# Optimization experiments

Measured on AMD Instinct MI355X. Metric: run time of the kernel, lower is better.

The kernel has to match this reference:

```python
import jax, jax.numpy as jnp
import numpy as np

N, E, G = 20000, 320000, 128
HID, HEADS, LAYERS, IN = 128, 4, 2, 74
EPS = 1e-5


def setup_inputs() -> dict:
    key = jax.random.key(0)
    ks = jax.random.split(key, 10)
    h = jax.random.normal(ks[0], (N, IN), dtype=jnp.float32)
    src = jax.random.randint(ks[1], (E,), 0, N, dtype=jnp.int32)
    dst = jax.random.randint(ks[2], (E,), 0, N, dtype=jnp.int32)
    graph_ids = jnp.sort(jax.random.randint(ks[3], (N,), 0, G, dtype=jnp.int32))
    W0 = jax.random.normal(ks[4], (HEADS, IN, HID), dtype=jnp.float32) / np.sqrt(IN)
    Wr = jax.random.normal(ks[5], (LAYERS - 1, HEADS, HID, HID), dtype=jnp.float32) / np.sqrt(HID)
    att = jax.random.normal(ks[6], (LAYERS, HEADS, 2 * HID), dtype=jnp.float32) / np.sqrt(2 * HID)
    gamma = jnp.ones((LAYERS, HEADS, HID), dtype=jnp.float32)
    beta = jnp.zeros((LAYERS, HEADS, HID), dtype=jnp.float32)
    out_w = jax.random.normal(ks[7], (LAYERS, HID), dtype=jnp.float32) / np.sqrt(HID)
    out_b = jnp.zeros((LAYERS,), dtype=jnp.float32)
    return {"h": h, "src": src, "dst": dst, "graph_ids": graph_ids,
            "W0": W0, "Wr": Wr, "att": att, "gamma": gamma, "beta": beta,
            "out_w": out_w, "out_b": out_b}


def _gat_head(h, W, a, g, b, src, dst):
    # h: [N, F_in], W: [F_in, HID], a: [2*HID]
    z = h @ W                                  # [N, HID]
    zs, zd = z[src], z[dst]                    # [E, HID] gathers
    e = jax.nn.leaky_relu(zs @ a[:HID] + zd @ a[HID:])  # [E] edge logits
    # segment softmax over incoming edges of each dst node
    emax = jax.ops.segment_max(e, dst, num_segments=N)
    ex = jnp.exp(e - emax[dst])
    denom = jax.ops.segment_sum(ex, dst, num_segments=N)
    alpha = ex / denom[dst]
    hout = jax.ops.segment_sum(alpha[:, None] * zs, dst, num_segments=N)  # [N, HID]
    r = jax.nn.relu(hout)
    # BatchNorm1d (training-mode batch stats, biased variance)
    mean = r.mean(0)
    var = r.var(0)
    return g * (r - mean) / jnp.sqrt(var + EPS) + b


def reference(h, src, dst, graph_ids, W0, Wr, att, gamma, beta, out_w, out_b):
    heads = jax.vmap(_gat_head, in_axes=(None, 0, 0, 0, 0, None, None))
    x = h
    for j in range(LAYERS):
        W = W0 if j == 0 else Wr[j - 1]
        hs = heads(x, W, att[j], gamma[j], beta[j], src, dst)  # [HEADS, N, HID]
        hs = jnp.transpose(hs, (1, 0, 2))                       # [N, HEADS, HID]
        score = jax.nn.softmax(hs @ out_w[j] + out_b[j], axis=1)  # [N, HEADS]
        x = jnp.einsum('nh,nhd->nd', score, hs)                 # [N, HID]
    # dgl.mean_nodes: per-graph mean of node features
    counts = jax.ops.segment_sum(jnp.ones((N,), dtype=x.dtype), graph_ids, num_segments=G)
    sums = jax.ops.segment_sum(x, graph_ids, num_segments=G)
    return sums / jnp.maximum(counts, 1.0)[:, None]
```

## Files before the change

kernel.cpp:

```cpp
#include <hip/hip_runtime.h>
#include <hip/hip_bf16.h>

typedef unsigned short u16;
typedef unsigned int u32;
typedef __attribute__((ext_vector_type(8))) short bf16x8;
typedef __attribute__((ext_vector_type(4))) float f32x4;

#define NN 20000
#define NE 320000
#define NG 128
#define HD 128
#define NH 4
#define KIN 74
#define KP0 96
#define BN_EPS 1e-5f

__device__ __forceinline__ float bf2f(u16 v){ return __uint_as_float(((u32)v)<<16); }
__device__ __forceinline__ float bflo(u32 v){ return __uint_as_float(v<<16); }
__device__ __forceinline__ float bfhi(u32 v){ return __uint_as_float(v & 0xffff0000u); }
__device__ __forceinline__ u16 f2bf(float f){
    u32 u = __float_as_uint(f);
    return (u16)((u + 0x7fffu + ((u>>16)&1u)) >> 16);
}
__device__ __forceinline__ u32 pack2(float a, float b){
    return (u32)f2bf(a) | ((u32)f2bf(b) << 16);
}

__global__ void k_hist(const int* __restrict__ dst, int* __restrict__ counts){
    int e = blockIdx.x*256 + threadIdx.x;
    if(e < NE) atomicAdd(&counts[dst[e]], 1);
}

__global__ void k_scan(const int* __restrict__ counts, int* __restrict__ rowptr,
                       int* __restrict__ cursor){
    __shared__ int wsum[16];
    int tx = threadIdx.x, lane = tx & 63, wid = tx >> 6;
    int running = 0;
    for(int t = 0; t < (NN + 1023)/1024; ++t){
        int i = t*1024 + tx;
        int v = (i < NN) ? counts[i] : 0;
        int s = v;
        #pragma unroll
        for(int d = 1; d < 64; d <<= 1){ int o = __shfl_up(s, d); if(lane >= d) s += o; }
        if(lane == 63) wsum[wid] = s;
        __syncthreads();
        int woff = 0, total = 0;
        for(int w_ = 0; w_ < 16; ++w_){ int sw = wsum[w_]; total += sw; if(w_ < wid) woff += sw; }
        int ex = running + woff + s - v;
        if(i < NN){ rowptr[i] = ex; cursor[i] = ex; }
        running += total;
        __syncthreads();
    }
    if(tx == 0) rowptr[NN] = running;
}

__global__ void k_scatter(const int* __restrict__ src, const int* __restrict__ dst,
                          int* __restrict__ cursor, int* __restrict__ srcs){
    int e = blockIdx.x*256 + threadIdx.x;
    if(e >= NE) return;
    int d = dst[e];
    int p = atomicAdd(&cursor[d], 1);
    srcs[p] = src[e];
}

__global__ void k_prep_h(const float* __restrict__ h, u16* __restrict__ hb){
    int i = blockIdx.x*256 + threadIdx.x;
    if(i >= NN*KP0) return;
    int n = i / KP0, k = i - n*KP0;
    hb[i] = (k < KIN) ? f2bf(h[n*KIN + k]) : (u16)0;
}

__global__ void k_prep_w0(const float* __restrict__ W0, u16* __restrict__ wt){
    int i = blockIdx.x*256 + threadIdx.x;
    if(i >= NH*HD*KP0) return;
    int k = i % KP0; int c = (i/KP0) % HD; int h = i/(KP0*HD);
    wt[i] = (k < KIN) ? f2bf(W0[(h*KIN + k)*HD + c]) : (u16)0;
}

__global__ void k_prep_w1(const float* __restrict__ Wr, u16* __restrict__ wt){
    int i = blockIdx.x*256 + threadIdx.x;
    if(i >= NH*HD*HD) return;
    int k = i % HD; int c = (i/HD) % HD; int h = i/(HD*HD);
    wt[i] = f2bf(Wr[(h*HD + k)*HD + c]);
}

template<int KP>
__global__ void k_gemm_mfma(const u16* __restrict__ xb, const u16* __restrict__ wt,
                            u16* __restrict__ z){
    int h = blockIdx.y;
    int tx = threadIdx.x, lane = tx & 63, w = tx >> 6;
    int n0 = blockIdx.x*32 + (w >> 1)*16;
    int c0 = (w & 1)*64;
    int r16 = lane & 15, kg = lane >> 4;
    const u16* ap = xb + (size_t)(n0 + r16)*KP + kg*8;
    const u16* bp = wt + ((size_t)h*HD + c0 + r16)*KP + kg*8;
    f32x4 acc0 = {0.f,0.f,0.f,0.f}, acc1 = {0.f,0.f,0.f,0.f};
    f32x4 acc2 = {0.f,0.f,0.f,0.f}, acc3 = {0.f,0.f,0.f,0.f};
    #pragma unroll
    for(int k0 = 0; k0 < KP; k0 += 32){
        bf16x8 av = *(const bf16x8*)(ap + k0);
        bf16x8 b0 = *(const bf16x8*)(bp + k0);
        bf16x8 b1 = *(const bf16x8*)(bp + 16*KP + k0);
        bf16x8 b2 = *(const bf16x8*)(bp + 32*KP + k0);
        bf16x8 b3 = *(const bf16x8*)(bp + 48*KP + k0);
        acc0 = __builtin_amdgcn_mfma_f32_16x16x32_bf16(av, b0, acc0, 0, 0, 0);
        acc1 = __builtin_amdgcn_mfma_f32_16x16x32_bf16(av, b1, acc1, 0, 0, 0);
        acc2 = __builtin_amdgcn_mfma_f32_16x16x32_bf16(av, b2, acc2, 0, 0, 0);
        acc3 = __builtin_amdgcn_mfma_f32_16x16x32_bf16(av, b3, acc3, 0, 0, 0);
    }
    int nbase = n0 + kg*4;
    u16* zp = z + ((size_t)nbase*NH + h)*HD + c0 + r16;
    #pragma unroll
    for(int reg = 0; reg < 4; ++reg){
        u16* q = zp + (size_t)reg*NH*HD;
        q[0]  = f2bf(acc0[reg]);
        q[16] = f2bf(acc1[reg]);
        q[32] = f2bf(acc2[reg]);
        q[48] = f2bf(acc3[reg]);
    }
}

__global__ void k_dots(const u16* __restrict__ z, const float* __restrict__ attj,
                       float* __restrict__ es, float* __restrict__ ed){
    int tx = threadIdx.x, lane = tx & 63, w = tx >> 6;
    int n = blockIdx.x*4 + w;
    if(n >= NN) return;
    int ch = lane*2;
    for(int h = 0; h < NH; ++h){
        u32 zz = *(const u32*)(z + (size_t)(n*NH + h)*HD + ch);
        float z0 = bflo(zz);
        float z1 = bfhi(zz);
        const float* a = attj + h*2*HD;
        float ps = z0*a[ch]    + z1*a[ch+1];
        float pd = z0*a[HD+ch] + z1*a[HD+ch+1];
        #pragma unroll
        for(int d = 32; d > 0; d >>= 1){ ps += __shfl_xor(ps, d); pd += __shfl_xor(pd, d); }
        if(lane == 0){ es[n*NH + h] = ps; ed[n*NH + h] = pd; }
    }
}

__global__ void k_aggregate(const int* __restrict__ rowptr, const int* __restrict__ srcs,
                            const float* __restrict__ es, const float* __restrict__ ed,
                            const u16* __restrict__ z, u16* __restrict__ r){
    int n = blockIdx.x;
    int tx = threadIdx.x, lane = tx & 63, h = tx >> 6;
    int p0 = rowptr[n], p1 = rowptr[n+1];
    int eslot = lane >> 4;
    int cidx  = lane & 15;
    float edn = ed[n*NH + h];
    float ssum = 0.f;
    float acc[8];
    #pragma unroll
    for(int k = 0; k < 8; ++k) acc[k] = 0.f;

    for(int base = p0; base < p1; base += 64){
        int p = base + lane;
        int sn = 0; float ex = 0.f;
        if(p < p1){
            sn = srcs[p];
            float e = es[sn*NH + h] + edn;
            e = e >= 0.f ? e : 0.01f*e;
            ex = __expf(e);
        }
        ssum += ex;
        int cnt = min(64, p1 - base);
        int niter = (cnt + 7) >> 3;
        for(int i = 0; i < niter; ++i){
            int e0 = i*8 + eslot;
            int e1 = e0 + 4;
            float a0 = __shfl(ex, e0);
            int   s0 = __shfl(sn, e0);
            float a1 = __shfl(ex, e1);
            int   s1 = __shfl(sn, e1);
            const uint4* q0 = (const uint4*)(z + (s0*NH + h)*HD + cidx*8);
            const uint4* q1 = (const uint4*)(z + (s1*NH + h)*HD + cidx*8);
            uint4 v0 = *q0;
            uint4 v1 = *q1;
            acc[0] += a0*bflo(v0.x); acc[1] += a0*bfhi(v0.x);
            acc[2] += a0*bflo(v0.y); acc[3] += a0*bfhi(v0.y);
            acc[4] += a0*bflo(v0.z); acc[5] += a0*bfhi(v0.z);
            acc[6] += a0*bflo(v0.w); acc[7] += a0*bfhi(v0.w);
            acc[0] += a1*bflo(v1.x); acc[1] += a1*bfhi(v1.x);
            acc[2] += a1*bflo(v1.y); acc[3] += a1*bfhi(v1.y);
            acc[4] += a1*bflo(v1.z); acc[5] += a1*bfhi(v1.z);
            acc[6] += a1*bflo(v1.w); acc[7] += a1*bfhi(v1.w);
        }
    }
    #pragma unroll
    for(int k = 0; k < 8; ++k){
        acc[k] += __shfl_xor(acc[k], 16);
        acc[k] += __shfl_xor(acc[k], 32);
    }
    #pragma unroll
    for(int d = 32; d > 0; d >>= 1) ssum += __shfl_xor(ssum, d);
    float inv = (ssum > 0.f) ? 1.f/ssum : 0.f;
    if(eslot == 0){
        float c0 = fmaxf(acc[0]*inv, 0.f), c1 = fmaxf(acc[1]*inv, 0.f);
        float c2 = fmaxf(acc[2]*inv, 0.f), c3 = fmaxf(acc[3]*inv, 0.f);
        float c4 = fmaxf(acc[4]*inv, 0.f), c5 = fmaxf(acc[5]*inv, 0.f);
        float c6 = fmaxf(acc[6]*inv, 0.f), c7 = fmaxf(acc[7]*inv, 0.f);
        uint4 o;
        o.x = pack2(c0, c1); o.y = pack2(c2, c3);
        o.z = pack2(c4, c5); o.w = pack2(c6, c7);
        *(uint4*)(r + (n*NH + h)*HD + cidx*8) = o;
    }
}

__global__ void k_bnreduce(const u16* __restrict__ r, float* __restrict__ bnsum,
                           float* __restrict__ bnsqs){
    int c = blockIdx.x*256 + threadIdx.x;
    int nbeg = blockIdx.y * 160;
    float s = 0.f, s2 = 0.f;
    for(int i = 0; i < 160; ++i){
        float v = bf2f(r[(size_t)(nbeg+i)*512 + c]);
        s += v; s2 += v*v;
    }
    atomicAdd(&bnsum[c], s);
    atomicAdd(&bnsqs[c], s2);
}

__global__ void k_bnfin(const float* __restrict__ bnsum, const float* __restrict__ bnsqs,
                        const float* __restrict__ gamma, const float* __restrict__ beta,
                        float* __restrict__ inv, float* __restrict__ shift){
    int c = blockIdx.x*256 + threadIdx.x;
    if(c >= 512) return;
    float mean = bnsum[c] * (1.f/NN);
    float var  = bnsqs[c] * (1.f/NN) - mean*mean;
    float iv = gamma[c] * rsqrtf(var + BN_EPS);
    inv[c] = iv;
    shift[c] = beta[c] - mean*iv;
}

__global__ void k_headmix(const u16* __restrict__ r, const float* __restrict__ inv,
                          const float* __restrict__ shift, const float* __restrict__ ow,
                          u16* __restrict__ x){
    int tx = threadIdx.x, lane = tx & 63, w = tx >> 6;
    int n = blockIdx.x*4 + w;
    if(n >= NN) return;
    int ch = lane*2;
    float rn[NH][2];
    float sc[NH];
    #pragma unroll
    for(int h = 0; h < NH; ++h){
        int c = h*HD + ch;
        u32 zz = *(const u32*)(r + (size_t)n*512 + c);
        float v0 = bflo(zz)*inv[c]   + shift[c];
        float v1 = bfhi(zz)*inv[c+1] + shift[c+1];
        rn[h][0] = v0; rn[h][1] = v1;
        float p = v0*ow[ch] + v1*ow[ch+1];
        #pragma unroll
        for(int d = 32; d > 0; d >>= 1) p += __shfl_xor(p, d);
        sc[h] = p;
    }
    float m = fmaxf(fmaxf(sc[0], sc[1]), fmaxf(sc[2], sc[3]));
    float e0 = __expf(sc[0]-m), e1 = __expf(sc[1]-m), e2 = __expf(sc[2]-m), e3 = __expf(sc[3]-m);
    float is = 1.f/(e0+e1+e2+e3);
    float x0 = (e0*rn[0][0] + e1*rn[1][0] + e2*rn[2][0] + e3*rn[3][0])*is;
    float x1 = (e0*rn[0][1] + e1*rn[1][1] + e2*rn[2][1] + e3*rn[3][1])*is;
    *(u32*)(x + (size_t)n*HD + ch) = pack2(x0, x1);
}

__global__ void k_gmean(const int* __restrict__ gid, const u16* __restrict__ x,
                        float* __restrict__ out){
    int g = blockIdx.x;
    int tx = threadIdx.x, lane = tx & 63, w = tx >> 6;
    int lo = 0, hi = NN;
    while(lo < hi){ int mid = (lo + hi) >> 1; if(gid[mid] < g) lo = mid + 1; else hi = mid; }
    int start = lo;
    hi = NN;
    while(lo < hi){ int mid = (lo + hi) >> 1; if(gid[mid] < g + 1) lo = mid + 1; else hi = mid; }
    int end = lo;
    float a0 = 0.f, a1 = 0.f;
    for(int n = start + w; n < end; n += 4){
        u32 zz = *(const u32*)(x + (size_t)n*HD + lane*2);
        a0 += bflo(zz);
        a1 += bfhi(zz);
    }
    __shared__ float sm[4][HD];
    sm[w][lane*2]     = a0;
    sm[w][lane*2 + 1] = a1;
    __syncthreads();
    if(tx < HD){
        float s = sm[0][tx] + sm[1][tx] + sm[2][tx] + sm[3][tx];
        float cnt = (float)(end - start);
        out[g*HD + tx] = s / fmaxf(cnt, 1.f);
    }
}

extern "C" void kernel_launch(void* const* d_in, const int* in_sizes, int n_in,
                              void* d_out, int out_size, void* d_ws, size_t ws_size,
                              hipStream_t stream){
    const float* h     = (const float*)d_in[0];
    const int*   src   = (const int*)  d_in[1];
    const int*   dst   = (const int*)  d_in[2];
    const int*   gid   = (const int*)  d_in[3];
    const float* W0    = (const float*)d_in[4];
    const float* Wr    = (const float*)d_in[5];
    const float* att   = (const float*)d_in[6];
    const float* gamma = (const float*)d_in[7];
    const float* beta  = (const float*)d_in[8];
    const float* ow    = (const float*)d_in[9];

    char* p = (char*)d_ws;
    auto alloc = [&](size_t bytes) -> void* {
        void* q = (void*)p;
        p += (bytes + 255) & ~(size_t)255;
        return q;
    };
    u16*   z      = (u16*)  alloc((size_t)NN*NH*HD*2);
    u16*   r      = (u16*)  alloc((size_t)NN*NH*HD*2);
    u16*   x      = (u16*)  alloc((size_t)NN*HD*2);
    u16*   hb     = (u16*)  alloc((size_t)NN*KP0*2);
    u16*   wt0    = (u16*)  alloc((size_t)NH*HD*KP0*2);
    u16*   wt1    = (u16*)  alloc((size_t)NH*HD*HD*2);
    float* es     = (float*)alloc((size_t)NN*NH*4);
    float* ed     = (float*)alloc((size_t)NN*NH*4);
    int*   counts = (int*)  alloc((size_t)NN*4);
    int*   rowptr = (int*)  alloc((size_t)(NN+1)*4);
    int*   cursor = (int*)  alloc((size_t)NN*4);
    int*   srcs   = (int*)  alloc((size_t)NE*4);
    float* bnsum  = (float*)alloc(1024*4);
    float* bnsqs  = bnsum + 512;
    float* bninv  = (float*)alloc(1024*4);
    float* bnshift= bninv + 512;

    k_prep_h <<<(NN*KP0+255)/256, 256, 0, stream>>>(h, hb);
    k_prep_w0<<<(NH*HD*KP0+255)/256, 256, 0, stream>>>(W0, wt0);
    k_prep_w1<<<(NH*HD*HD+255)/256, 256, 0, stream>>>(Wr, wt1);

    hipMemsetAsync(counts, 0, (size_t)NN*4, stream);
    k_hist   <<<(NE+255)/256, 256, 0, stream>>>(dst, counts);
    k_scan   <<<1, 1024, 0, stream>>>(counts, rowptr, cursor);
    k_scatter<<<(NE+255)/256, 256, 0, stream>>>(src, dst, cursor, srcs);

    for(int j = 0; j < 2; ++j){
        if(j == 0) k_gemm_mfma<KP0><<<dim3(NN/32, NH), 256, 0, stream>>>(hb, wt0, z);
        else       k_gemm_mfma<HD> <<<dim3(NN/32, NH), 256, 0, stream>>>(x,  wt1, z);

        k_dots     <<<NN/4, 256, 0, stream>>>(z, att + j*NH*2*HD, es, ed);
        k_aggregate<<<NN, 256, 0, stream>>>(rowptr, srcs, es, ed, z, r);

        hipMemsetAsync(bnsum, 0, 1024*4, stream);
        k_bnreduce <<<dim3(2,125), 256, 0, stream>>>(r, bnsum, bnsqs);
        k_bnfin    <<<2, 256, 0, stream>>>(bnsum, bnsqs, gamma + j*512, beta + j*512,
                                           bninv, bnshift);
        k_headmix  <<<NN/4, 256, 0, stream>>>(r, bninv, bnshift, ow + j*HD, x);
    }

    k_gmean<<<NG, 256, 0, stream>>>(gid, x, (float*)d_out);
}
```

Before: 292.0 us.

## Store z head-major and map one wave per node-head in aggregation

The GEMM now writes z in [head][node][channel] order, and es/ed are stored per head. The dots and aggregate kernels gain a head grid dimension so each wave handles one (node, head) pair. The aggregate kernel drops the 64-edge shuffle batching and instead has each 16-lane group load its own edge directly, eight edges per step. The intent is better gather locality within a head's slice of z and fewer wasted lanes at average degree 16. In exchange, each edge's logit and exp are computed redundantly across 16 lanes, and the softmax denominator is rescaled by 16 to compensate.

```diff
diff --git a/kernel.cpp b/kernel.cpp
--- a/kernel.cpp
+++ b/kernel.cpp
@@ -5,6 +5,7 @@
 typedef unsigned int u32;
 typedef __attribute__((ext_vector_type(8))) short bf16x8;
 typedef __attribute__((ext_vector_type(4))) float f32x4;
+typedef __attribute__((ext_vector_type(2))) float f32x2;
 
 #define NN 20000
 #define NE 320000
@@ -109,10 +110,10 @@
         acc3 = __builtin_amdgcn_mfma_f32_16x16x32_bf16(av, b3, acc3, 0, 0, 0);
     }
     int nbase = n0 + kg*4;
-    u16* zp = z + ((size_t)nbase*NH + h)*HD + c0 + r16;
+    u16* zp = z + ((size_t)h*NN + nbase)*HD + c0 + r16;
     #pragma unroll
     for(int reg = 0; reg < 4; ++reg){
-        u16* q = zp + (size_t)reg*NH*HD;
+        u16* q = zp + (size_t)reg*HD;
         q[0]  = f2bf(acc0[reg]);
         q[16] = f2bf(acc1[reg]);
         q[32] = f2bf(acc2[reg]);
@@ -124,85 +125,82 @@
                        float* __restrict__ es, float* __restrict__ ed){
     int tx = threadIdx.x, lane = tx & 63, w = tx >> 6;
     int n = blockIdx.x*4 + w;
-    if(n >= NN) return;
+    int h = blockIdx.y;
     int ch = lane*2;
-    for(int h = 0; h < NH; ++h){
-        u32 zz = *(const u32*)(z + (size_t)(n*NH + h)*HD + ch);
-        float z0 = bflo(zz);
-        float z1 = bfhi(zz);
-        const float* a = attj + h*2*HD;
-        float ps = z0*a[ch]    + z1*a[ch+1];
-        float pd = z0*a[HD+ch] + z1*a[HD+ch+1];
-        #pragma unroll
-        for(int d = 32; d > 0; d >>= 1){ ps += __shfl_xor(ps, d); pd += __shfl_xor(pd, d); }
-        if(lane == 0){ es[n*NH + h] = ps; ed[n*NH + h] = pd; }
-    }
+    u32 zz = *(const u32*)(z + ((size_t)h*NN + n)*HD + ch);
+    float z0 = bflo(zz), z1 = bfhi(zz);
+    const float* a = attj + h*2*HD;
+    float ps = z0*a[ch]    + z1*a[ch+1];
+    float pd = z0*a[HD+ch] + z1*a[HD+ch+1];
+    #pragma unroll
+    for(int d = 32; d > 0; d >>= 1){ ps += __shfl_xor(ps, d); pd += __shfl_xor(pd, d); }
+    if(lane == 0){ es[(size_t)h*NN + n] = ps; ed[(size_t)h*NN + n] = pd; }
 }
 
 __global__ void k_aggregate(const int* __restrict__ rowptr, const int* __restrict__ srcs,
                             const float* __restrict__ es, const float* __restrict__ ed,
                             const u16* __restrict__ z, u16* __restrict__ r){
-    int n = blockIdx.x;
-    int tx = threadIdx.x, lane = tx & 63, h = tx >> 6;
+    int tx = threadIdx.x, lane = tx & 63, w = tx >> 6;
+    int n = blockIdx.x*4 + w;
+    int h = blockIdx.y;
     int p0 = rowptr[n], p1 = rowptr[n+1];
     int eslot = lane >> 4;
     int cidx  = lane & 15;
-    float edn = ed[n*NH + h];
+    const float* esh = es + (size_t)h*NN;
+    const u16*   zh  = z  + (size_t)h*NN*HD;
+    float edn = ed[(size_t)h*NN + n];
     float ssum = 0.f;
-    float acc[8];
-    #pragma unroll
-    for(int k = 0; k < 8; ++k) acc[k] = 0.f;
-
-    for(int base = p0; base < p1; base += 64){
-        int p = base + lane;
-        int sn = 0; float ex = 0.f;
-        if(p < p1){
-            sn = srcs[p];
-            float e = es[sn*NH + h] + edn;
+    f32x2 acc[4];
+    #pragma unroll
+    for(int k = 0; k < 4; ++k) acc[k] = (f32x2){0.f, 0.f};
+
+    for(int base = p0; base < p1; base += 8){
+        int q0 = base + eslot, q1 = q0 + 4;
+        int s0 = 0, s1 = 0;
+        float ex0 = 0.f, ex1 = 0.f;
+        if(q0 < p1){
+            s0 = srcs[q0];
+            float e = esh[s0] + edn;
             e = e >= 0.f ? e : 0.01f*e;
-            ex = __expf(e);
+            ex0 = __expf(e);
         }
-        ssum += ex;
-        int cnt = min(64, p1 - base);
-        int niter = (cnt + 7) >> 3;
-        for(int i = 0; i < niter; ++i){
-            int e0 = i*8 + eslot;
-            int e1 = e0 + 4;
-            float a0 = __shfl(ex, e0);
-            int   s0 = __shfl(sn, e0);
-            float a1 = __shfl(ex, e1);
-            int   s1 = __shfl(sn, e1);
-            const uint4* q0 = (const uint4*)(z + (s0*NH + h)*HD + cidx*8);
-            const uint4* q1 = (const uint4*)(z + (s1*NH + h)*HD + cidx*8);
-            uint4 v0 = *q0;
-            uint4 v1 = *q1;
-            acc[0] += a0*bflo(v0.x); acc[1] += a0*bfhi(v0.x);
-            acc[2] += a0*bflo(v0.y); acc[3] += a0*bfhi(v0.y);
-            acc[4] += a0*bflo(v0.z); acc[5] += a0*bfhi(v0.z);
-            acc[6] += a0*bflo(v0.w); acc[7] += a0*bfhi(v0.w);
-            acc[0] += a1*bflo(v1.x); acc[1] += a1*bfhi(v1.x);
-            acc[2] += a1*bflo(v1.y); acc[3] += a1*bfhi(v1.y);
-            acc[4] += a1*bflo(v1.z); acc[5] += a1*bfhi(v1.z);
-            acc[6] += a1*bflo(v1.w); acc[7] += a1*bfhi(v1.w);
+        if(q1 < p1){
+            s1 = srcs[q1];
+            float e = esh[s1] + edn;
+            e = e >= 0.f ? e : 0.01f*e;
+            ex1 = __expf(e);
         }
-    }
-    #pragma unroll
-    for(int k = 0; k < 8; ++k){
-        acc[k] += __shfl_xor(acc[k], 16);
-        acc[k] += __shfl_xor(acc[k], 32);
+        ssum += ex0 + ex1;
+        uint4 v0 = *(const uint4*)(zh + (size_t)s0*HD + cidx*8);
+        uint4 v1 = *(const uint4*)(zh + (size_t)s1*HD + cidx*8);
+        f32x2 t;
+        t.x = bflo(v0.x); t.y = bfhi(v0.x); acc[0] += ex0*t;
+        t.x = bflo(v0.y); t.y = bfhi(v0.y); acc[1] += ex0*t;
+        t.x = bflo(v0.z); t.y = bfhi(v0.z); acc[2] += ex0*t;
+        t.x = bflo(v0.w); t.y = bfhi(v0.w); acc[3] += ex0*t;
+        t.x = bflo(v1.x); t.y = bfhi(v1.x); acc[0] += ex1*t;
+        t.x = bflo(v1.y); t.y = bfhi(v1.y); acc[1] += ex1*t;
+        t.x = bflo(v1.z); t.y = bfhi(v1.z); acc[2] += ex1*t;
+        t.x = bflo(v1.w); t.y = bfhi(v1.w); acc[3] += ex1*t;
+    }
+    float c01[8];
+    #pragma unroll
+    for(int k = 0; k < 4; ++k){
+        float a0 = acc[k].x, a1 = acc[k].y;
+        a0 += __shfl_xor(a0, 16); a0 += __shfl_xor(a0, 32);
+        a1 += __shfl_xor(a1, 16); a1 += __shfl_xor(a1, 32);
+        c01[k*2] = a0; c01[k*2+1] = a1;
     }
     #pragma unroll
     for(int d = 32; d > 0; d >>= 1) ssum += __shfl_xor(ssum, d);
-    float inv = (ssum > 0.f) ? 1.f/ssum : 0.f;
+    float inv = (ssum > 0.f) ? 16.f/ssum : 0.f;
     if(eslot == 0){
-        float c0 = fmaxf(acc[0]*inv, 0.f), c1 = fmaxf(acc[1]*inv, 0.f);
-        float c2 = fmaxf(acc[2]*inv, 0.f), c3 = fmaxf(acc[3]*inv, 0.f);
-        float c4 = fmaxf(acc[4]*inv, 0.f), c5 = fmaxf(acc[5]*inv, 0.f);
-        float c6 = fmaxf(acc[6]*inv, 0.f), c7 = fmaxf(acc[7]*inv, 0.f);
         uint4 o;
-        o.x = pack2(c0, c1); o.y = pack2(c2, c3);
-        o.z = pack2(c4, c5); o.w = pack2(c6, c7);
-        *(uint4*)(r + (n*NH + h)*HD + cidx*8) = o;
+        o.x = pack2(fmaxf(c01[0]*inv, 0.f), fmaxf(c01[1]*inv, 0.f));
+        o.y = pack2(fmaxf(c01[2]*inv, 0.f), fmaxf(c01[3]*inv, 0.f));
+        o.z = pack2(fmaxf(c01[4]*inv, 0.f), fmaxf(c01[5]*inv, 0.f));
+        o.w = pack2(fmaxf(c01[6]*inv, 0.f), fmaxf(c01[7]*inv, 0.f));
+        *(uint4*)(r + ((size_t)n*NH + h)*HD + cidx*8) = o;
     }
 }
 
@@ -337,8 +335,8 @@
         if(j == 0) k_gemm_mfma<KP0><<<dim3(NN/32, NH), 256, 0, stream>>>(hb, wt0, z);
         else       k_gemm_mfma<HD> <<<dim3(NN/32, NH), 256, 0, stream>>>(x,  wt1, z);
 
-        k_dots     <<<NN/4, 256, 0, stream>>>(z, att + j*NH*2*HD, es, ed);
-        k_aggregate<<<NN, 256, 0, stream>>>(rowptr, srcs, es, ed, z, r);
+        k_dots     <<<dim3(NN/4, NH), 256, 0, stream>>>(z, att + j*NH*2*HD, es, ed);
+        k_aggregate<<<dim3(NN/4, NH), 256, 0, stream>>>(rowptr, srcs, es, ed, z, r);
 
         hipMemsetAsync(bnsum, 0, 1024*4, stream);
         k_bnreduce <<<dim3(2,125), 256, 0, stream>>>(r, bnsum, bnsqs);
```

Result: slower. 315.3 us (+8.0%).
